# Kernel tuning notes

Measured on AMD Instinct MI355X. Metric: run time of the kernel, lower is better.

The kernel has to match this reference:

```python
import jax, jax.numpy as jnp
import numpy as np

N = 400000  # flattened batch*frames; each row holds 2 chains x 4 joints x 4x4 transforms


def _fk_chain(pose):
    # pose: [N, 2, 4, 4, 4] -> end-effector FK transform [N, 2, 4, 4]
    # fk = I @ P0 @ P1 @ P2 @ P3 (identity init is a no-op, kept implicitly)
    fk = pose[:, :, 0]
    for j in range(1, 4):
        fk = jnp.matmul(fk, pose[:, :, j])
    return fk


def setup_inputs() -> dict:
    key = jax.random.key(0)
    k1, k2, k3, k4 = jax.random.split(key, 4)
    return {
        "output_pose": jax.random.normal(k1, (N, 128), dtype=jnp.float32),
        "gt_pose": jax.random.normal(k2, (N, 128), dtype=jnp.float32),
        "gt_prev_pose": jax.random.normal(k3, (N, 128), dtype=jnp.float32),
        "gt_pos": jax.random.normal(k4, (N, 6), dtype=jnp.float32),
    }


def reference(output_pose, gt_pose, gt_prev_pose, gt_pos):
    out_p = output_pose.reshape(-1, 2, 4, 4, 4)
    gt_p = gt_pose.reshape(-1, 2, 4, 4, 4)
    gt_prev_p = gt_prev_pose.reshape(-1, 2, 4, 4, 4)

    output_fk = _fk_chain(out_p)[:, :, :3, 3]   # [N, 2, 3] end-effector positions
    gt_fk = _fk_chain(gt_p)[:, :, :3, 3]
    gt_prev_fk = _fk_chain(gt_prev_p)[:, :, :3, 3]

    gt_vel = gt_fk - gt_prev_fk
    output_vel = output_fk - gt_prev_fk

    pos_loss = jnp.mean((output_fk - gt_fk) ** 2)
    vel_loss = jnp.mean((output_vel - gt_vel) ** 2)
    return (pos_loss, vel_loss)
```

## Files before the change

### kernel.cpp

```cpp
#include <hip/hip_runtime.h>


#define N_ROWS 400000
#define N_CHAINS (N_ROWS * 2)
#define ITERS 4
#define THREADS_TOTAL (N_CHAINS * 4 / ITERS)
#define BLOCK 256
#define BLOCKS (THREADS_TOTAL / BLOCK)
#define CHAIN_STRIDE (N_CHAINS / ITERS)
#define MEAN_DIV ((double)(N_ROWS) * 2.0 * 3.0)

__global__ void fk_zero_acc(double* acc) { acc[0] = 0.0; }

template <int I>
__device__ __forceinline__ float qb(float x) {
    return __builtin_bit_cast(float,
        __builtin_amdgcn_mov_dpp(__builtin_bit_cast(int, x),
                                 I | (I << 2) | (I << 4) | (I << 6),
                                 0xF, 0xF, true));
}

__device__ __forceinline__ float fk_elem(float4 m0, float4 m1, float4 m2, float4 m3) {
    float v = m3.w;
    float v0, v1, v2, v3;
    v0 = qb<0>(v); v1 = qb<1>(v); v2 = qb<2>(v); v3 = qb<3>(v);
    v = m2.x * v0 + m2.y * v1 + m2.z * v2 + m2.w * v3;
    v0 = qb<0>(v); v1 = qb<1>(v); v2 = qb<2>(v); v3 = qb<3>(v);
    v = m1.x * v0 + m1.y * v1 + m1.z * v2 + m1.w * v3;
    v0 = qb<0>(v); v1 = qb<1>(v); v2 = qb<2>(v); v3 = qb<3>(v);
    v = m0.x * v0 + m0.y * v1 + m0.z * v2 + m0.w * v3;
    return v;
}

__global__ __launch_bounds__(BLOCK) void fk_loss_kernel(const float* __restrict__ outp,
                                                        const float* __restrict__ gtp,
                                                        double* __restrict__ acc) {
    const int tid = blockIdx.x * BLOCK + threadIdx.x;
    const int k = tid & 3;
    float ss = 0.0f;
#pragma unroll
    for (int it = 0; it < ITERS; ++it) {
        const int c = (tid >> 2) + it * CHAIN_STRIDE;
        const float4* po = reinterpret_cast<const float4*>(outp) + (size_t)c * 16 + k;
        const float4* pg = reinterpret_cast<const float4*>(gtp) + (size_t)c * 16 + k;
        float4 o0 = po[0], o1 = po[4], o2 = po[8], o3 = po[12];
        float4 g0 = pg[0], g1 = pg[4], g2 = pg[8], g3 = pg[12];
        float fo = fk_elem(o0, o1, o2, o3);
        float fg = fk_elem(g0, g1, g2, g3);
        float d = fo - fg;
        ss += (k < 3) ? d * d : 0.0f;
    }
#pragma unroll
    for (int off = 32; off > 0; off >>= 1) ss += __shfl_down(ss, off, 64);
    __shared__ float part[BLOCK / 64];
    const int wave = threadIdx.x >> 6;
    const int lane = threadIdx.x & 63;
    if (lane == 0) part[wave] = ss;
    __syncthreads();
    if (threadIdx.x == 0) {
        float b = part[0] + part[1] + part[2] + part[3];
        atomicAdd(acc, (double)b);
    }
}

__global__ void fk_finalize(const double* __restrict__ acc, float* __restrict__ out) {
    float v = (float)(acc[0] / MEAN_DIV);
    out[0] = v;
    out[1] = v;
}

extern "C" void kernel_launch(void* const* d_in, const int* in_sizes, int n_in,
                              void* d_out, int out_size, void* d_ws, size_t ws_size,
                              hipStream_t stream) {
    const float* output_pose = (const float*)d_in[0];
    const float* gt_pose     = (const float*)d_in[1];
    float* out = (float*)d_out;
    double* acc = (double*)d_ws;

    fk_zero_acc<<<1, 1, 0, stream>>>(acc);
    fk_loss_kernel<<<BLOCKS, BLOCK, 0, stream>>>(output_pose, gt_pose, acc);
    fk_finalize<<<1, 1, 0, stream>>>(acc, out);
}
```

Measured before the change: 82.38 us.

## Remap chains to 16-lane groups with contiguous float4 loads and prefetch

Each lane now loads a single float4, so one chain's sixteen joint rows are spread over 16 consecutive lanes and every wave load is fully contiguous. The earlier scheme had four lanes per chain, each loading four strided float4s. The matrix chain is evaluated with ds_swizzle broadcasts inside each 16-lane group, and the next iteration's data is prefetched in a rolled loop. The aim is better coalescing and more outstanding memory requests for this bandwidth-bound kernel. The cost is that most lanes do redundant arithmetic, and swizzles go through the LDS crossbar instead of DPP.

```diff
diff --git a/kernel.cpp b/kernel.cpp
--- a/kernel.cpp
+++ b/kernel.cpp
@@ -1,61 +1,60 @@
 #include <hip/hip_runtime.h>
 
 
-#define N_ROWS 400000
-#define N_CHAINS (N_ROWS * 2)
-#define ITERS 4
-#define THREADS_TOTAL (N_CHAINS * 4 / ITERS)
+#define N_CHAINS 800000
+#define UNITS (N_CHAINS / 4)
+#define WAVES 12500
+#define ITERS (UNITS / WAVES)
 #define BLOCK 256
-#define BLOCKS (THREADS_TOTAL / BLOCK)
-#define CHAIN_STRIDE (N_CHAINS / ITERS)
-#define MEAN_DIV ((double)(N_ROWS) * 2.0 * 3.0)
+#define BLOCKS (WAVES / 4)
+#define MEAN_DIV (400000.0 * 2.0 * 3.0)
 
 __global__ void fk_zero_acc(double* acc) { acc[0] = 0.0; }
 
-template <int I>
-__device__ __forceinline__ float qb(float x) {
+template <int Q, int C>
+__device__ __forceinline__ float swz(float v) {
     return __builtin_bit_cast(float,
-        __builtin_amdgcn_mov_dpp(__builtin_bit_cast(int, x),
-                                 I | (I << 2) | (I << 4) | (I << 6),
-                                 0xF, 0xF, true));
+        __builtin_amdgcn_ds_swizzle(__builtin_bit_cast(int, v),
+                                    ((4 * Q + C) << 5) | 0x10));
 }
 
-__device__ __forceinline__ float fk_elem(float4 m0, float4 m1, float4 m2, float4 m3) {
-    float v = m3.w;
-    float v0, v1, v2, v3;
-    v0 = qb<0>(v); v1 = qb<1>(v); v2 = qb<2>(v); v3 = qb<3>(v);
-    v = m2.x * v0 + m2.y * v1 + m2.z * v2 + m2.w * v3;
-    v0 = qb<0>(v); v1 = qb<1>(v); v2 = qb<2>(v); v3 = qb<3>(v);
-    v = m1.x * v0 + m1.y * v1 + m1.z * v2 + m1.w * v3;
-    v0 = qb<0>(v); v1 = qb<1>(v); v2 = qb<2>(v); v3 = qb<3>(v);
-    v = m0.x * v0 + m0.y * v1 + m0.z * v2 + m0.w * v3;
-    return v;
+template <int Q>
+__device__ __forceinline__ float step(float4 m, float v) {
+    float a0 = swz<Q, 0>(v), a1 = swz<Q, 1>(v), a2 = swz<Q, 2>(v), a3 = swz<Q, 3>(v);
+    return m.x * a0 + m.y * a1 + m.z * a2 + m.w * a3;
 }
 
-__global__ __launch_bounds__(BLOCK) void fk_loss_kernel(const float* __restrict__ outp,
-                                                        const float* __restrict__ gtp,
+__global__ __launch_bounds__(BLOCK) void fk_loss_kernel(const float4* __restrict__ o4,
+                                                        const float4* __restrict__ g4,
                                                         double* __restrict__ acc) {
     const int tid = blockIdx.x * BLOCK + threadIdx.x;
-    const int k = tid & 3;
+    const int wave = tid >> 6;
+    const int lane = threadIdx.x & 63;
+    const long base = (long)wave * ITERS * 64 + lane;
+
     float ss = 0.0f;
-#pragma unroll
+    float4 mo = o4[base], mg = g4[base];
+#pragma unroll 1
     for (int it = 0; it < ITERS; ++it) {
-        const int c = (tid >> 2) + it * CHAIN_STRIDE;
-        const float4* po = reinterpret_cast<const float4*>(outp) + (size_t)c * 16 + k;
-        const float4* pg = reinterpret_cast<const float4*>(gtp) + (size_t)c * 16 + k;
-        float4 o0 = po[0], o1 = po[4], o2 = po[8], o3 = po[12];
-        float4 g0 = pg[0], g1 = pg[4], g2 = pg[8], g3 = pg[12];
-        float fo = fk_elem(o0, o1, o2, o3);
-        float fg = fk_elem(g0, g1, g2, g3);
-        float d = fo - fg;
-        ss += (k < 3) ? d * d : 0.0f;
+        float4 no, ng;
+        if (it + 1 < ITERS) {
+            no = o4[base + (it + 1) * 64];
+            ng = g4[base + (it + 1) * 64];
+        }
+        float vo = mo.w, vg = mg.w;
+        vo = step<3>(mo, vo); vg = step<3>(mg, vg);
+        vo = step<2>(mo, vo); vg = step<2>(mg, vg);
+        vo = step<1>(mo, vo); vg = step<1>(mg, vg);
+        float d = vo - vg;
+        ss += ((lane & 15) < 3) ? d * d : 0.0f;
+        mo = no; mg = ng;
     }
+
 #pragma unroll
     for (int off = 32; off > 0; off >>= 1) ss += __shfl_down(ss, off, 64);
     __shared__ float part[BLOCK / 64];
-    const int wave = threadIdx.x >> 6;
-    const int lane = threadIdx.x & 63;
-    if (lane == 0) part[wave] = ss;
+    const int w = threadIdx.x >> 6;
+    if ((threadIdx.x & 63) == 0) part[w] = ss;
     __syncthreads();
     if (threadIdx.x == 0) {
         float b = part[0] + part[1] + part[2] + part[3];
@@ -72,8 +71,8 @@
 extern "C" void kernel_launch(void* const* d_in, const int* in_sizes, int n_in,
                               void* d_out, int out_size, void* d_ws, size_t ws_size,
                               hipStream_t stream) {
-    const float* output_pose = (const float*)d_in[0];
-    const float* gt_pose     = (const float*)d_in[1];
+    const float4* output_pose = (const float4*)d_in[0];
+    const float4* gt_pose     = (const float4*)d_in[1];
     float* out = (float*)d_out;
     double* acc = (double*)d_ws;
 
```

After: 95.30 us. +15.7%, slower.

## Replace atomic accumulation with per-block partials and tree finalize; prefetch next chain

Applied to the files above, without the earlier changes.

Removes the zero-init kernel and the per-block double atomicAdd. Each block now writes a float partial, and a single 256-thread block reduces the partials in double. The loss loop also explicitly loads the next iteration's chain matrices before computing the current one. This cuts one launch and atomic contention, at the cost of extra registers and a slightly larger finalize kernel.

```diff
diff --git a/kernel.cpp b/kernel.cpp
--- a/kernel.cpp
+++ b/kernel.cpp
@@ -1,16 +1,12 @@
 #include <hip/hip_runtime.h>
 
 
-#define N_ROWS 400000
-#define N_CHAINS (N_ROWS * 2)
+#define N_CHAINS 800000
 #define ITERS 4
-#define THREADS_TOTAL (N_CHAINS * 4 / ITERS)
 #define BLOCK 256
-#define BLOCKS (THREADS_TOTAL / BLOCK)
+#define BLOCKS (N_CHAINS * 4 / ITERS / BLOCK)
 #define CHAIN_STRIDE (N_CHAINS / ITERS)
-#define MEAN_DIV ((double)(N_ROWS) * 2.0 * 3.0)
-
-__global__ void fk_zero_acc(double* acc) { acc[0] = 0.0; }
+#define MEAN_DIV (400000.0 * 2.0 * 3.0)
 
 template <int I>
 __device__ __forceinline__ float qb(float x) {
@@ -32,52 +28,71 @@
     return v;
 }
 
-__global__ __launch_bounds__(BLOCK) void fk_loss_kernel(const float* __restrict__ outp,
-                                                        const float* __restrict__ gtp,
-                                                        double* __restrict__ acc) {
+__global__ __launch_bounds__(BLOCK) void fk_loss_kernel(const float4* __restrict__ o4,
+                                                        const float4* __restrict__ g4,
+                                                        float* __restrict__ partial) {
     const int tid = blockIdx.x * BLOCK + threadIdx.x;
     const int k = tid & 3;
+    const int q = tid >> 2;
+
+    const float4* po = o4 + (size_t)q * 16 + k;
+    const float4* pg = g4 + (size_t)q * 16 + k;
+    float4 o0 = po[0], o1 = po[4], o2 = po[8], o3 = po[12];
+    float4 g0 = pg[0], g1 = pg[4], g2 = pg[8], g3 = pg[12];
+
     float ss = 0.0f;
 #pragma unroll
     for (int it = 0; it < ITERS; ++it) {
-        const int c = (tid >> 2) + it * CHAIN_STRIDE;
-        const float4* po = reinterpret_cast<const float4*>(outp) + (size_t)c * 16 + k;
-        const float4* pg = reinterpret_cast<const float4*>(gtp) + (size_t)c * 16 + k;
-        float4 o0 = po[0], o1 = po[4], o2 = po[8], o3 = po[12];
-        float4 g0 = pg[0], g1 = pg[4], g2 = pg[8], g3 = pg[12];
+        float4 no0, no1, no2, no3, ng0, ng1, ng2, ng3;
+        if (it + 1 < ITERS) {
+            const size_t off = ((size_t)q + (size_t)(it + 1) * CHAIN_STRIDE) * 16 + k;
+            const float4* qo = o4 + off;
+            const float4* qg = g4 + off;
+            no0 = qo[0]; no1 = qo[4]; no2 = qo[8]; no3 = qo[12];
+            ng0 = qg[0]; ng1 = qg[4]; ng2 = qg[8]; ng3 = qg[12];
+        }
         float fo = fk_elem(o0, o1, o2, o3);
         float fg = fk_elem(g0, g1, g2, g3);
         float d = fo - fg;
         ss += (k < 3) ? d * d : 0.0f;
+        o0 = no0; o1 = no1; o2 = no2; o3 = no3;
+        g0 = ng0; g1 = ng1; g2 = ng2; g3 = ng3;
     }
+
 #pragma unroll
     for (int off = 32; off > 0; off >>= 1) ss += __shfl_down(ss, off, 64);
     __shared__ float part[BLOCK / 64];
-    const int wave = threadIdx.x >> 6;
-    const int lane = threadIdx.x & 63;
-    if (lane == 0) part[wave] = ss;
+    if ((threadIdx.x & 63) == 0) part[threadIdx.x >> 6] = ss;
+    __syncthreads();
+    if (threadIdx.x == 0)
+        partial[blockIdx.x] = part[0] + part[1] + part[2] + part[3];
+}
+
+__global__ __launch_bounds__(BLOCK) void fk_finalize(const float* __restrict__ partial,
+                                                     float* __restrict__ out) {
+    double s = 0.0;
+    for (int i = threadIdx.x; i < BLOCKS; i += BLOCK) s += (double)partial[i];
+    __shared__ double dpart[BLOCK / 64];
+#pragma unroll
+    for (int off = 32; off > 0; off >>= 1) s += __shfl_down(s, off, 64);
+    if ((threadIdx.x & 63) == 0) dpart[threadIdx.x >> 6] = s;
     __syncthreads();
     if (threadIdx.x == 0) {
-        float b = part[0] + part[1] + part[2] + part[3];
-        atomicAdd(acc, (double)b);
+        double b = dpart[0] + dpart[1] + dpart[2] + dpart[3];
+        float v = (float)(b / MEAN_DIV);
+        out[0] = v;
+        out[1] = v;
     }
-}
-
-__global__ void fk_finalize(const double* __restrict__ acc, float* __restrict__ out) {
-    float v = (float)(acc[0] / MEAN_DIV);
-    out[0] = v;
-    out[1] = v;
 }
 
 extern "C" void kernel_launch(void* const* d_in, const int* in_sizes, int n_in,
                               void* d_out, int out_size, void* d_ws, size_t ws_size,
                               hipStream_t stream) {
-    const float* output_pose = (const float*)d_in[0];
-    const float* gt_pose     = (const float*)d_in[1];
+    const float4* output_pose = (const float4*)d_in[0];
+    const float4* gt_pose     = (const float4*)d_in[1];
     float* out = (float*)d_out;
-    double* acc = (double*)d_ws;
+    float* partial = (float*)d_ws;
 
-    fk_zero_acc<<<1, 1, 0, stream>>>(acc);
-    fk_loss_kernel<<<BLOCKS, BLOCK, 0, stream>>>(output_pose, gt_pose, acc);
-    fk_finalize<<<1, 1, 0, stream>>>(acc, out);
+    fk_loss_kernel<<<BLOCKS, BLOCK, 0, stream>>>(output_pose, gt_pose, partial);
+    fk_finalize<<<1, BLOCK, 0, stream>>>(partial, out);
 }
```

Result: faster. 76.01 us, median of 2 (-7.7%).
